# Performance work log

Hardware: AMD Instinct MI355X
Metric: run time of the kernel (lower is better)

## Reference

```python
import jax, jax.numpy as jnp
import numpy as np


def setup_inputs() -> dict:
    key = jax.random.key(0)
    ks = jax.random.split(key, 7)
    B, S = 64, 1024
    V, E, H, L, O = 128, 512, 512, 2, 256
    scale = 0.05
    return {
        "input_ids": jax.random.randint(ks[0], (B, S), 0, V),
        "emb": jax.random.normal(ks[1], (V, E), dtype=jnp.float32) * scale,
        "Wxh": jax.random.normal(ks[2], (L, H, E), dtype=jnp.float32) * scale,
        "Whh": jax.random.normal(ks[3], (L, H, H), dtype=jnp.float32) * scale,
        "bh": jax.random.normal(ks[4], (L, H), dtype=jnp.float32) * scale,
        "Why": jax.random.normal(ks[5], (O, H), dtype=jnp.float32) * scale,
        "by": jax.random.normal(ks[6], (O,), dtype=jnp.float32) * scale,
    }


def reference(input_ids, emb, Wxh, Whh, bh, Why, by):
    # input_ids: [B, S] int; emb: [V, E]; Wxh/Whh: [L, H, *]; bh: [L, H]
    L, H, _ = Wxh.shape
    B, S = input_ids.shape
    embedded = emb[input_ids]                 # [B, S, E]
    xs = jnp.swapaxes(embedded, 0, 1)         # [S, B, E] for scan over time
    h0 = jnp.zeros((L, B, H), dtype=embedded.dtype)

    def step(h, x_t):
        inp = x_t
        new_h = []
        for l in range(L):  # small fixed layer loop
            hn = jnp.tanh(inp @ Wxh[l].T + h[l] @ Whh[l].T + bh[l])
            new_h.append(hn)
            inp = hn
        return jnp.stack(new_h), inp          # carry [L,B,H], emit top layer [B,H]

    _, ys = jax.lax.scan(step, h0, xs)        # ys: [S, B, H]
    hidden_seq = jnp.swapaxes(ys, 0, 1)       # [B, S, H]
    return hidden_seq @ Why.T + by            # [B, S, O]
```

## Files before the change

kernel.cpp:

```cpp
#include <hip/hip_runtime.h>
#include <stdint.h>

#define B_ 64
#define S_ 1024
#define V_ 128
#define E_ 512
#define H_ 512
#define O_ 256
#define SLOTU 32768

typedef __attribute__((ext_vector_type(8))) short bf16x8;
typedef __attribute__((ext_vector_type(4))) float f32x4;
typedef __attribute__((ext_vector_type(4))) unsigned int u32x4;
typedef __attribute__((ext_vector_type(2))) unsigned int u32x2;
typedef unsigned short u16;
typedef unsigned int u32;

__device__ __forceinline__ u16 f2bf(float f) {
  unsigned u = __builtin_bit_cast(unsigned, f);
  u = u + 0x7FFFu + ((u >> 16) & 1u);
  return (u16)(u >> 16);
}
__device__ __forceinline__ float bf2f(u16 h) {
  unsigned u = ((unsigned)h) << 16;
  return __builtin_bit_cast(float, u);
}
__device__ __forceinline__ float fast_tanh(float x) {
  float a = __builtin_amdgcn_exp2f(x * 2.8853900817779268f);
  return 1.0f - 2.0f * __builtin_amdgcn_rcpf(a + 1.0f);
}
__device__ __forceinline__ u32 pk_hi(u32 a, u32 b) { return (a & 0xffffu) | (b << 16); }
__device__ __forceinline__ u32 pk_lo(u32 a, u32 b) { return (a >> 16) | (b & 0xffff0000u); }

__device__ __forceinline__ u32x4 ld_sc1_x4(const u32* p) {
  u32x4 v;
  asm volatile("global_load_dwordx4 %0, %1, off sc0 sc1" : "=v"(v) : "v"(p));
  return v;
}
__device__ __forceinline__ u32 ld_sc1_u32(const u32* p) {
  u32 v;
  asm volatile("global_load_dword %0, %1, off sc0 sc1" : "=v"(v) : "v"(p));
  return v;
}
__device__ __forceinline__ void st_sc1_u32(u32* p, u32 v) {
  asm volatile("global_store_dword %0, %1, off sc0 sc1" :: "v"(p), "v"(v) : "memory");
}
__device__ __forceinline__ void st_short_nt(u16* p, u32 v) {
  asm volatile("global_store_short %0, %1, off nt" :: "v"(p), "v"(v) : "memory");
}
__device__ __forceinline__ void vm0_fence() {
  asm volatile("s_waitcnt vmcnt(0)" ::: "memory");
  __builtin_amdgcn_sched_barrier(0);
}
__device__ __forceinline__ void poll4(const u32* p, u32 tgt) {
  for (;;) {
    u32x4 v;
    asm volatile("global_load_dwordx4 %0, %1, off sc0 sc1\n\ts_waitcnt vmcnt(0)"
                 : "=v"(v) : "v"(p) : "memory");
    if (v.x >= tgt && v.y >= tgt && v.z >= tgt && v.w >= tgt) return;
    __builtin_amdgcn_s_sleep(1);
  }
}

__global__ void k_embed(const float* __restrict__ emb, const float* __restrict__ Wxh0,
                        const float* __restrict__ bh0, float* __restrict__ EW0) {
  __shared__ float es[E_];
  const int v = blockIdx.x;
  for (int e = threadIdx.x; e < E_; e += blockDim.x) es[e] = emb[v * E_ + e];
  __syncthreads();
  for (int h = threadIdx.x; h < H_; h += blockDim.x) {
    const float* wr = Wxh0 + (size_t)h * E_;
    float acc = bh0[h];
    #pragma unroll 4
    for (int e = 0; e < E_; e += 4)
      acc += es[e] * wr[e] + es[e+1] * wr[e+1] + es[e+2] * wr[e+2] + es[e+3] * wr[e+3];
    EW0[(size_t)v * H_ + h] = acc;
  }
}

__global__ __launch_bounds__(512, 2) void k_pipe(
    const float* __restrict__ Whh, const float* __restrict__ Wxh,
    const int* __restrict__ ids, const float* __restrict__ EW0,
    const float* __restrict__ bh,
    u32* __restrict__ h0r,
    u32* __restrict__ x1r,
    u32* __restrict__ h1r,
    u16* __restrict__ h1full,
    u32* __restrict__ fa)
{
  __shared__ u32 lds_hi_w[2 * 4096];
  __shared__ u32 lds_lo_w[2 * 4096];

  const int tid  = threadIdx.x;
  const int wave = tid >> 6, lane = tid & 63;
  const int l15 = lane & 15, lhi = lane >> 4;
  const int bid = blockIdx.x;
  const int role = bid >> 4, sub = bid & 15;
  const int g = sub >> 2, cb = sub & 3;
  const int n = cb * 128 + wave * 16 + l15;
  const int goff = g * 16 * 512;

  u32* h0f = fa;
  u32* x1f = fa + 256;
  u32* h1f = fa + 512;

  const float* Wsel = (role == 0) ? Whh
                    : (role == 1) ? (Wxh + (size_t)H_ * H_)
                                  : (Whh + (size_t)H_ * H_);
  bf16x8 whi[16], wlo[16];
  {
    const float* wr = Wsel + (size_t)n * H_ + lhi * 8;
    #pragma unroll
    for (int ks = 0; ks < 16; ++ks) {
      const float* src = wr + ks * 32;
      bf16x8 h, l;
      #pragma unroll
      for (int j = 0; j < 8; ++j) {
        const float v = src[j];
        const u16 hb = f2bf(v);
        h[j] = (short)hb;
        l[j] = (short)f2bf(v - bf2f(hb));
      }
      whi[ks] = h; wlo[ks] = l;
    }
  }

  int aoff[16];
  {
    const int sw = l15 & 7;
    #pragma unroll
    for (int ks = 0; ks < 16; ++ks)
      aoff[ks] = l15 * 1024 + (((ks * 4 + lhi) ^ sw) << 4);
  }

  const int sr = tid >> 5, sm = tid & 31;
  auto stage_wr = [&](int buf, int cs, u32x4 q) {
    const int byte = buf * 16384 + sr * 1024 + (sm & 1) * 8 +
                     ((((cs << 4) + (sm >> 1)) ^ (sr & 7)) << 4);
    u32x2 hi = { pk_hi(q.x, q.y), pk_hi(q.z, q.w) };
    u32x2 lo = { pk_lo(q.x, q.y), pk_lo(q.z, q.w) };
    *(u32x2*)((char*)lds_hi_w + byte) = hi;
    *(u32x2*)((char*)lds_lo_w + byte) = lo;
  };
  auto stage3 = [&](const u32* base, int buf) {
    const u32* rowp = base + sr * 512 + sm * 4;
    const int c0 = (cb + 1) & 3, c1 = (cb + 2) & 3, c2 = (cb + 3) & 3;
    u32x4 q0 = ld_sc1_x4(rowp + c0 * 128);
    u32x4 q1 = ld_sc1_x4(rowp + c1 * 128);
    u32x4 q2 = ld_sc1_x4(rowp + c2 * 128);
    vm0_fence();
    stage_wr(buf, c0, q0); stage_wr(buf, c1, q1); stage_wr(buf, c2, q2);
  };
  auto stage4 = [&](const u32* base, int buf) {
    const u32* rowp = base + sr * 512 + sm * 4;
    u32x4 q0 = ld_sc1_x4(rowp);
    u32x4 q1 = ld_sc1_x4(rowp + 128);
    u32x4 q2 = ld_sc1_x4(rowp + 256);
    u32x4 q3 = ld_sc1_x4(rowp + 384);
    vm0_fence();
    stage_wr(buf, 0, q0); stage_wr(buf, 1, q1); stage_wr(buf, 2, q2); stage_wr(buf, 3, q3);
  };

  auto mm3 = [&](int buf, f32x4& out) {
    const char* bh_ = (const char*)lds_hi_w + buf * 16384;
    const char* bl_ = (const char*)lds_lo_w + buf * 16384;
    f32x4 c0 = {0.f,0.f,0.f,0.f}, c1 = c0, c2 = c0;
    #pragma unroll
    for (int ks = 0; ks < 16; ++ks) {
      bf16x8 ah = *(const bf16x8*)(bh_ + aoff[ks]);
      bf16x8 al = *(const bf16x8*)(bl_ + aoff[ks]);
      c0 = __builtin_amdgcn_mfma_f32_16x16x32_bf16(ah, whi[ks], c0, 0, 0, 0);
      c1 = __builtin_amdgcn_mfma_f32_16x16x32_bf16(al, whi[ks], c1, 0, 0, 0);
      c2 = __builtin_amdgcn_mfma_f32_16x16x32_bf16(ah, wlo[ks], c2, 0, 0, 0);
    }
    out = c0 + c1 + c2;
  };

  auto self_write = [&](int buf, const u16* hbv, const u16* lbv) {
    char* bh_ = (char*)lds_hi_w + buf * 16384;
    char* bl_ = (char*)lds_lo_w + buf * 16384;
    const int gcol = n >> 3, coff = (n & 7) * 2;
    #pragma unroll
    for (int j = 0; j < 4; ++j) {
      const int r = lhi * 4 + j;
      const int byte = r * 1024 + ((gcol ^ (r & 7)) << 4) + coff;
      *(u16*)(bh_ + byte) = hbv[j];
      *(u16*)(bl_ + byte) = lbv[j];
    }
  };

  if (role == 0) {
    for (int t = 0; t < S_; ++t) {
      float ew[4];
      #pragma unroll
      for (int j = 0; j < 4; ++j) {
        const int b = g * 16 + lhi * 4 + j;
        ew[j] = EW0[(size_t)ids[b * S_ + t] * H_ + n];
      }
      if (tid == 0) {
        if (t > 0) poll4(&h0f[((g << 4) | ((t - 1) & 15)) * 4], (u32)t);
        if ((t & 7) == 0 && t >= 16)
          poll4(&x1f[((g << 4) | ((t - 9) & 15)) * 4], (u32)(t - 8));
      }
      __syncthreads();
      const int cur = t & 1;
      f32x4 acc = {0.f,0.f,0.f,0.f};
      if (t > 0) {
        stage3(h0r + (size_t)((t - 1) & 15) * SLOTU + goff, cur);
        __syncthreads();
        mm3(cur, acc);
      }
      u32* wsl = h0r + (size_t)(t & 15) * SLOTU;
      u16 hbv[4], lbv[4];
      #pragma unroll
      for (int j = 0; j < 4; ++j) {
        const int b = g * 16 + lhi * 4 + j;
        const float h = fast_tanh(acc[j] + ew[j]);
        hbv[j] = f2bf(h);
        lbv[j] = f2bf(h - bf2f(hbv[j]));
        st_sc1_u32(wsl + (size_t)b * 512 + n, (u32)hbv[j] | ((u32)lbv[j] << 16));
      }
      self_write(cur ^ 1, hbv, lbv);
      vm0_fence();
      __syncthreads();
      if (tid == 0) st_sc1_u32(&h0f[((g << 4) | (t & 15)) * 4 + cb], (u32)(t + 1));
    }
  } else if (role == 1) {
    const float bias = bh[H_ + n];
    for (int t = 0; t < S_; ++t) {
      if (tid == 0) {
        poll4(&h0f[((g << 4) | (t & 15)) * 4], (u32)(t + 1));
        if ((t & 7) == 0 && t >= 16)
          poll4(&h1f[((g << 4) | ((t - 9) & 15)) * 4], (u32)(t - 8));
      }
      __syncthreads();
      const int cur = t & 1;
      stage4(h0r + (size_t)(t & 15) * SLOTU + goff, cur);
      __syncthreads();
      f32x4 acc;
      mm3(cur, acc);
      u32* xsl = x1r + (size_t)(t & 15) * SLOTU;
      #pragma unroll
      for (int j = 0; j < 4; ++j) {
        const int b = g * 16 + lhi * 4 + j;
        const float v = acc[j] + bias;
        st_sc1_u32(xsl + (size_t)b * 512 + n, __builtin_bit_cast(u32, v));
      }
      vm0_fence();
      __syncthreads();
      if (tid == 0) st_sc1_u32(&x1f[((g << 4) | (t & 15)) * 4 + cb], (u32)(t + 1));
    }
  } else {
    for (int t = 0; t < S_; ++t) {
      if (tid == 0) {
        poll4(&x1f[((g << 4) | (t & 15)) * 4], (u32)(t + 1));
        if (t > 0) poll4(&h1f[((g << 4) | ((t - 1) & 15)) * 4], (u32)t);
      }
      __syncthreads();
      const u32* xsl = x1r + (size_t)(t & 15) * SLOTU;
      u32 xv[4];
      #pragma unroll
      for (int j = 0; j < 4; ++j) {
        const int b = g * 16 + lhi * 4 + j;
        xv[j] = ld_sc1_u32(xsl + (size_t)b * 512 + n);
      }
      const int cur = t & 1;
      f32x4 acc = {0.f,0.f,0.f,0.f};
      if (t > 0) {
        stage3(h1r + (size_t)((t - 1) & 3) * SLOTU + goff, cur);
        __syncthreads();
        mm3(cur, acc);
        vm0_fence();
      } else {
        vm0_fence();
      }
      u32* wsl = h1r + (size_t)(t & 3) * SLOTU;
      u16 hbv[4], lbv[4];
      #pragma unroll
      for (int j = 0; j < 4; ++j) {
        const int b = g * 16 + lhi * 4 + j;
        const float h = fast_tanh(acc[j] + __builtin_bit_cast(float, xv[j]));
        hbv[j] = f2bf(h);
        lbv[j] = f2bf(h - bf2f(hbv[j]));
        st_sc1_u32(wsl + (size_t)b * 512 + n, (u32)hbv[j] | ((u32)lbv[j] << 16));
      }
      self_write(cur ^ 1, hbv, lbv);
      vm0_fence();
      __syncthreads();
      if (tid == 0) st_sc1_u32(&h1f[((g << 4) | (t & 15)) * 4 + cb], (u32)(t + 1));
      #pragma unroll
      for (int j = 0; j < 4; ++j) {
        const int b = g * 16 + lhi * 4 + j;
        st_short_nt(h1full + ((size_t)b * S_ + t) * H_ + n, (u32)hbv[j]);
      }
    }
  }
}

__global__ void k_gemm_out(const u16* __restrict__ A, const float* __restrict__ Bw,
                           const float* __restrict__ bias, float* __restrict__ outp) {
  const int tid  = threadIdx.x;
  const int wave = tid >> 6, lane = tid & 63;
  const int l15 = lane & 15, lhi = lane >> 4;
  const int M0  = blockIdx.x * 64;
  const int ncb = wave * 64;

  #pragma unroll
  for (int nt = 0; nt < 4; ++nt) {
    const int nn = ncb + nt * 16 + l15;
    const float* wr = Bw + (size_t)nn * H_ + lhi * 8;
    bf16x8 w[16];
    #pragma unroll
    for (int ks = 0; ks < 16; ++ks) {
      const float* src = wr + ks * 32;
      bf16x8 ww;
      #pragma unroll
      for (int j = 0; j < 8; ++j) ww[j] = (short)f2bf(src[j]);
      w[ks] = ww;
    }
    const float bs = bias[nn];
    for (int mi = 0; mi < 4; ++mi) {
      const int m0 = M0 + mi * 16;
      const u16* arow = A + ((size_t)(m0 + l15)) * H_ + lhi * 8;
      f32x4 acc = {0.f, 0.f, 0.f, 0.f};
      #pragma unroll
      for (int ks = 0; ks < 16; ++ks) {
        bf16x8 a = *(const bf16x8*)(arow + ks * 32);
        acc = __builtin_amdgcn_mfma_f32_16x16x32_bf16(a, w[ks], acc, 0, 0, 0);
      }
      #pragma unroll
      for (int j = 0; j < 4; ++j)
        outp[(size_t)(m0 + lhi * 4 + j) * O_ + nn] = acc[j] + bs;
    }
  }
}

extern "C" void kernel_launch(void* const* d_in, const int* in_sizes, int n_in,
                              void* d_out, int out_size, void* d_ws, size_t ws_size,
                              hipStream_t stream) {
  const int*   ids = (const int*)d_in[0];
  const float* emb = (const float*)d_in[1];
  const float* Wxh = (const float*)d_in[2];
  const float* Whh = (const float*)d_in[3];
  const float* bh  = (const float*)d_in[4];
  const float* Why = (const float*)d_in[5];
  const float* by  = (const float*)d_in[6];
  float* out = (float*)d_out;

  char* ws = (char*)d_ws;
  size_t off = 0;
  float* EW0  = (float*)(ws + off); off += (size_t)V_ * H_ * 4;
  u32* h0r    = (u32*)(ws + off);   off += (size_t)16 * SLOTU * 4;
  u32* x1r    = (u32*)(ws + off);   off += (size_t)16 * SLOTU * 4;
  u32* h1r    = (u32*)(ws + off);   off += (size_t)4 * SLOTU * 4;
  u32* fa     = (u32*)(ws + off);   off += 4096;
  u16* h1full = (u16*)(ws + off);   off += (size_t)B_ * S_ * H_ * 2;

  hipMemsetAsync(fa, 0, 4096, stream);

  k_embed<<<dim3(V_), dim3(256), 0, stream>>>(emb, Wxh, bh, EW0);

  k_pipe<<<dim3(48), dim3(512), 0, stream>>>(Whh, Wxh, ids, EW0, bh,
                                             h0r, x1r, h1r, h1full, fa);

  k_gemm_out<<<dim3((B_ * S_) / 64), dim3(256), 0, stream>>>(h1full, Why, by, out);
}
```

Before: 3.931 ms.

## Replace flag-based inter-block sync with per-element sequence tags on data

Each hidden-state element is now stored together with a step tag in a dwordx2, and consumers poll the data itself until every tag matches, instead of waiting on separate per-step flag words after a vmcnt fence and block barrier. This removes one round trip of flag store and flag poll per timestep in all three pipeline roles, and drops several __syncthreads. Coarse progress counters are kept only for ring-buffer backpressure, published every 8 steps. It also reorders the loops so the next step's state is staged right after this step's output. The cost is doubled ring-buffer traffic, a larger memset to clear the tags, and spin loops executed by every thread.

New measurement: 4.188 ms. +6.5%, slower.

```diff
diff --git a/kernel.cpp b/kernel.cpp
--- a/kernel.cpp
+++ b/kernel.cpp
@@ -7,7 +7,7 @@
 #define E_ 512
 #define H_ 512
 #define O_ 256
-#define SLOTU 32768
+#define PSLOT (B_ * H_ * 2)
 
 typedef __attribute__((ext_vector_type(8))) short bf16x8;
 typedef __attribute__((ext_vector_type(4))) float f32x4;
@@ -37,10 +37,14 @@
   asm volatile("global_load_dwordx4 %0, %1, off sc0 sc1" : "=v"(v) : "v"(p));
   return v;
 }
-__device__ __forceinline__ u32 ld_sc1_u32(const u32* p) {
-  u32 v;
-  asm volatile("global_load_dword %0, %1, off sc0 sc1" : "=v"(v) : "v"(p));
+__device__ __forceinline__ u32x2 ld_sc1_x2(const u32* p) {
+  u32x2 v;
+  asm volatile("global_load_dwordx2 %0, %1, off sc0 sc1" : "=v"(v) : "v"(p));
   return v;
+}
+__device__ __forceinline__ void st_sc1_x2(u32* p, u32 d, u32 tag) {
+  u32x2 v = {d, tag};
+  asm volatile("global_store_dwordx2 %0, %1, off sc0 sc1" :: "v"(p), "v"(v) : "memory");
 }
 __device__ __forceinline__ void st_sc1_u32(u32* p, u32 v) {
   asm volatile("global_store_dword %0, %1, off sc0 sc1" :: "v"(p), "v"(v) : "memory");
@@ -98,11 +102,9 @@
   const int role = bid >> 4, sub = bid & 15;
   const int g = sub >> 2, cb = sub & 3;
   const int n = cb * 128 + wave * 16 + l15;
-  const int goff = g * 16 * 512;
-
-  u32* h0f = fa;
-  u32* x1f = fa + 256;
-  u32* h1f = fa + 512;
+
+  u32* x1prog = fa;
+  u32* r2prog = fa + 16;
 
   const float* Wsel = (role == 0) ? Whh
                     : (role == 1) ? (Wxh + (size_t)H_ * H_)
@@ -134,31 +136,56 @@
   }
 
   const int sr = tid >> 5, sm = tid & 31;
-  auto stage_wr = [&](int buf, int cs, u32x4 q) {
+  const int rowbase = (g * 16 + sr) * 512;
+
+  auto wr_lds = [&](int buf, int cs, u32 d0, u32 d1, u32 d2, u32 d3) {
     const int byte = buf * 16384 + sr * 1024 + (sm & 1) * 8 +
                      ((((cs << 4) + (sm >> 1)) ^ (sr & 7)) << 4);
-    u32x2 hi = { pk_hi(q.x, q.y), pk_hi(q.z, q.w) };
-    u32x2 lo = { pk_lo(q.x, q.y), pk_lo(q.z, q.w) };
+    u32x2 hi = { pk_hi(d0, d1), pk_hi(d2, d3) };
+    u32x2 lo = { pk_lo(d0, d1), pk_lo(d2, d3) };
     *(u32x2*)((char*)lds_hi_w + byte) = hi;
     *(u32x2*)((char*)lds_lo_w + byte) = lo;
   };
-  auto stage3 = [&](const u32* base, int buf) {
-    const u32* rowp = base + sr * 512 + sm * 4;
+
+  auto pollstage3 = [&](const u32* slot, u32 want, int buf) {
     const int c0 = (cb + 1) & 3, c1 = (cb + 2) & 3, c2 = (cb + 3) & 3;
-    u32x4 q0 = ld_sc1_x4(rowp + c0 * 128);
-    u32x4 q1 = ld_sc1_x4(rowp + c1 * 128);
-    u32x4 q2 = ld_sc1_x4(rowp + c2 * 128);
-    vm0_fence();
-    stage_wr(buf, c0, q0); stage_wr(buf, c1, q1); stage_wr(buf, c2, q2);
+    const u32* p0 = slot + ((rowbase + c0 * 128 + sm * 4) << 1);
+    const u32* p1 = slot + ((rowbase + c1 * 128 + sm * 4) << 1);
+    const u32* p2 = slot + ((rowbase + c2 * 128 + sm * 4) << 1);
+    u32x4 a0, a1, b0, b1, d0, d1;
+    for (;;) {
+      a0 = ld_sc1_x4(p0); a1 = ld_sc1_x4(p0 + 4);
+      b0 = ld_sc1_x4(p1); b1 = ld_sc1_x4(p1 + 4);
+      d0 = ld_sc1_x4(p2); d1 = ld_sc1_x4(p2 + 4);
+      vm0_fence();
+      u32 bad = (a0.y ^ want) | (a0.w ^ want) | (a1.y ^ want) | (a1.w ^ want)
+              | (b0.y ^ want) | (b0.w ^ want) | (b1.y ^ want) | (b1.w ^ want)
+              | (d0.y ^ want) | (d0.w ^ want) | (d1.y ^ want) | (d1.w ^ want);
+      if (!bad) break;
+    }
+    wr_lds(buf, c0, a0.x, a0.z, a1.x, a1.z);
+    wr_lds(buf, c1, b0.x, b0.z, b1.x, b1.z);
+    wr_lds(buf, c2, d0.x, d0.z, d1.x, d1.z);
   };
-  auto stage4 = [&](const u32* base, int buf) {
-    const u32* rowp = base + sr * 512 + sm * 4;
-    u32x4 q0 = ld_sc1_x4(rowp);
-    u32x4 q1 = ld_sc1_x4(rowp + 128);
-    u32x4 q2 = ld_sc1_x4(rowp + 256);
-    u32x4 q3 = ld_sc1_x4(rowp + 384);
-    vm0_fence();
-    stage_wr(buf, 0, q0); stage_wr(buf, 1, q1); stage_wr(buf, 2, q2); stage_wr(buf, 3, q3);
+
+  auto pollstage4 = [&](const u32* slot, u32 want, int buf) {
+    const u32* p0 = slot + ((rowbase + sm * 4) << 1);
+    u32x4 q[8];
+    for (;;) {
+      #pragma unroll
+      for (int c = 0; c < 4; ++c) {
+        q[2*c]   = ld_sc1_x4(p0 + (c * 128 << 1));
+        q[2*c+1] = ld_sc1_x4(p0 + (c * 128 << 1) + 4);
+      }
+      vm0_fence();
+      u32 bad = 0;
+      #pragma unroll
+      for (int i = 0; i < 8; ++i) bad |= (q[i].y ^ want) | (q[i].w ^ want);
+      if (!bad) break;
+    }
+    #pragma unroll
+    for (int c = 0; c < 4; ++c)
+      wr_lds(buf, c, q[2*c].x, q[2*c].z, q[2*c+1].x, q[2*c+1].z);
   };
 
   auto mm3 = [&](int buf, f32x4& out) {
@@ -197,20 +224,10 @@
         const int b = g * 16 + lhi * 4 + j;
         ew[j] = EW0[(size_t)ids[b * S_ + t] * H_ + n];
       }
-      if (tid == 0) {
-        if (t > 0) poll4(&h0f[((g << 4) | ((t - 1) & 15)) * 4], (u32)t);
-        if ((t & 7) == 0 && t >= 16)
-          poll4(&x1f[((g << 4) | ((t - 9) & 15)) * 4], (u32)(t - 8));
-      }
-      __syncthreads();
       const int cur = t & 1;
       f32x4 acc = {0.f,0.f,0.f,0.f};
-      if (t > 0) {
-        stage3(h0r + (size_t)((t - 1) & 15) * SLOTU + goff, cur);
-        __syncthreads();
-        mm3(cur, acc);
-      }
-      u32* wsl = h0r + (size_t)(t & 15) * SLOTU;
+      if (t > 0) mm3(cur, acc);
+      u32* wsl = h0r + (size_t)(t & 15) * PSLOT;
       u16 hbv[4], lbv[4];
       #pragma unroll
       for (int j = 0; j < 4; ++j) {
@@ -218,81 +235,104 @@
         const float h = fast_tanh(acc[j] + ew[j]);
         hbv[j] = f2bf(h);
         lbv[j] = f2bf(h - bf2f(hbv[j]));
-        st_sc1_u32(wsl + (size_t)b * 512 + n, (u32)hbv[j] | ((u32)lbv[j] << 16));
+        st_sc1_x2(wsl + (((size_t)b * 512 + n) << 1),
+                  (u32)hbv[j] | ((u32)lbv[j] << 16), (u32)(t + 1));
       }
       self_write(cur ^ 1, hbv, lbv);
-      vm0_fence();
+      if ((t & 7) == 0 && t >= 16 && tid == 0) poll4(&x1prog[g * 4], (u32)(t - 8));
+      if (t + 1 < S_) pollstage3(wsl, (u32)(t + 1), cur ^ 1);
       __syncthreads();
-      if (tid == 0) st_sc1_u32(&h0f[((g << 4) | (t & 15)) * 4 + cb], (u32)(t + 1));
     }
   } else if (role == 1) {
     const float bias = bh[H_ + n];
     for (int t = 0; t < S_; ++t) {
-      if (tid == 0) {
-        poll4(&h0f[((g << 4) | (t & 15)) * 4], (u32)(t + 1));
-        if ((t & 7) == 0 && t >= 16)
-          poll4(&h1f[((g << 4) | ((t - 9) & 15)) * 4], (u32)(t - 8));
-      }
-      __syncthreads();
+      if ((t & 7) == 0 && t >= 16 && tid == 0) poll4(&r2prog[g * 4], (u32)(t - 8));
       const int cur = t & 1;
-      stage4(h0r + (size_t)(t & 15) * SLOTU + goff, cur);
+      pollstage4(h0r + (size_t)(t & 15) * PSLOT, (u32)(t + 1), cur);
       __syncthreads();
       f32x4 acc;
       mm3(cur, acc);
-      u32* xsl = x1r + (size_t)(t & 15) * SLOTU;
+      u32* xsl = x1r + (size_t)(t & 15) * PSLOT;
       #pragma unroll
       for (int j = 0; j < 4; ++j) {
         const int b = g * 16 + lhi * 4 + j;
         const float v = acc[j] + bias;
-        st_sc1_u32(xsl + (size_t)b * 512 + n, __builtin_bit_cast(u32, v));
-      }
-      vm0_fence();
-      __syncthreads();
-      if (tid == 0) st_sc1_u32(&x1f[((g << 4) | (t & 15)) * 4 + cb], (u32)(t + 1));
+        st_sc1_x2(xsl + (((size_t)b * 512 + n) << 1),
+                  __builtin_bit_cast(u32, v), (u32)(t + 1));
+      }
+      if ((t & 7) == 7 && tid == 0) st_sc1_u32(&x1prog[g * 4 + cb], (u32)(t + 1));
     }
   } else {
+    u32 xvb[4];
+    {
+      const u32* xsl = x1r;
+      u32x2 xq[4];
+      for (;;) {
+        #pragma unroll
+        for (int j = 0; j < 4; ++j) {
+          const int b = g * 16 + lhi * 4 + j;
+          xq[j] = ld_sc1_x2(xsl + (((size_t)b * 512 + n) << 1));
+        }
+        vm0_fence();
+        u32 bad = 0;
+        #pragma unroll
+        for (int j = 0; j < 4; ++j) bad |= xq[j].y ^ 1u;
+        if (!bad) break;
+      }
+      #pragma unroll
+      for (int j = 0; j < 4; ++j) xvb[j] = xq[j].x;
+    }
     for (int t = 0; t < S_; ++t) {
-      if (tid == 0) {
-        poll4(&x1f[((g << 4) | (t & 15)) * 4], (u32)(t + 1));
-        if (t > 0) poll4(&h1f[((g << 4) | ((t - 1) & 15)) * 4], (u32)t);
-      }
-      __syncthreads();
-      const u32* xsl = x1r + (size_t)(t & 15) * SLOTU;
-      u32 xv[4];
+      const int cur = t & 1;
+      f32x4 acc = {0.f,0.f,0.f,0.f};
+      if (t > 0) mm3(cur, acc);
+      u32* wsl = h1r + (size_t)(t & 3) * PSLOT;
+      u16 hbv[4], lbv[4];
       #pragma unroll
       for (int j = 0; j < 4; ++j) {
         const int b = g * 16 + lhi * 4 + j;
-        xv[j] = ld_sc1_u32(xsl + (size_t)b * 512 + n);
-      }
-      const int cur = t & 1;
-      f32x4 acc = {0.f,0.f,0.f,0.f};
-      if (t > 0) {
-        stage3(h1r + (size_t)((t - 1) & 3) * SLOTU + goff, cur);
-        __syncthreads();
-        mm3(cur, acc);
-        vm0_fence();
-      } else {
-        vm0_fence();
-      }
-      u32* wsl = h1r + (size_t)(t & 3) * SLOTU;
-      u16 hbv[4], lbv[4];
-      #pragma unroll
-      for (int j = 0; j < 4; ++j) {
-        const int b = g * 16 + lhi * 4 + j;
-        const float h = fast_tanh(acc[j] + __builtin_bit_cast(float, xv[j]));
+        const float h = fast_tanh(acc[j] + __builtin_bit_cast(float, xvb[j]));
         hbv[j] = f2bf(h);
         lbv[j] = f2bf(h - bf2f(hbv[j]));
-        st_sc1_u32(wsl + (size_t)b * 512 + n, (u32)hbv[j] | ((u32)lbv[j] << 16));
+        st_sc1_x2(wsl + (((size_t)b * 512 + n) << 1),
+                  (u32)hbv[j] | ((u32)lbv[j] << 16), (u32)(t + 1));
+        st_short_nt(h1full + ((size_t)b * S_ + t) * H_ + n, (u32)hbv[j]);
       }
       self_write(cur ^ 1, hbv, lbv);
-      vm0_fence();
+      if ((t & 7) == 7 && tid == 0) st_sc1_u32(&r2prog[g * 4 + cb], (u32)(t + 1));
+      if (t + 1 < S_) {
+        const u32 want = (u32)(t + 1), xwant = (u32)(t + 2);
+        const int c0 = (cb + 1) & 3, c1 = (cb + 2) & 3, c2 = (cb + 3) & 3;
+        const u32* p0 = wsl + ((rowbase + c0 * 128 + sm * 4) << 1);
+        const u32* p1 = wsl + ((rowbase + c1 * 128 + sm * 4) << 1);
+        const u32* p2 = wsl + ((rowbase + c2 * 128 + sm * 4) << 1);
+        const u32* xsl = x1r + (size_t)((t + 1) & 15) * PSLOT;
+        u32x4 a0, a1, b0, b1, d0, d1;
+        u32x2 xq[4];
+        for (;;) {
+          a0 = ld_sc1_x4(p0); a1 = ld_sc1_x4(p0 + 4);
+          b0 = ld_sc1_x4(p1); b1 = ld_sc1_x4(p1 + 4);
+          d0 = ld_sc1_x4(p2); d1 = ld_sc1_x4(p2 + 4);
+          #pragma unroll
+          for (int j = 0; j < 4; ++j) {
+            const int b = g * 16 + lhi * 4 + j;
+            xq[j] = ld_sc1_x2(xsl + (((size_t)b * 512 + n) << 1));
+          }
+          vm0_fence();
+          u32 bad = (a0.y ^ want) | (a0.w ^ want) | (a1.y ^ want) | (a1.w ^ want)
+                  | (b0.y ^ want) | (b0.w ^ want) | (b1.y ^ want) | (b1.w ^ want)
+                  | (d0.y ^ want) | (d0.w ^ want) | (d1.y ^ want) | (d1.w ^ want);
+          #pragma unroll
+          for (int j = 0; j < 4; ++j) bad |= xq[j].y ^ xwant;
+          if (!bad) break;
+        }
+        wr_lds(cur ^ 1, c0, a0.x, a0.z, a1.x, a1.z);
+        wr_lds(cur ^ 1, c1, b0.x, b0.z, b1.x, b1.z);
+        wr_lds(cur ^ 1, c2, d0.x, d0.z, d1.x, d1.z);
+        #pragma unroll
+        for (int j = 0; j < 4; ++j) xvb[j] = xq[j].x;
+      }
       __syncthreads();
-      if (tid == 0) st_sc1_u32(&h1f[((g << 4) | (t & 15)) * 4 + cb], (u32)(t + 1));
-      #pragma unroll
-      for (int j = 0; j < 4; ++j) {
-        const int b = g * 16 + lhi * 4 + j;
-        st_short_nt(h1full + ((size_t)b * S_ + t) * H_ + n, (u32)hbv[j]);
-      }
     }
   }
 }
@@ -350,13 +390,14 @@
   char* ws = (char*)d_ws;
   size_t off = 0;
   float* EW0  = (float*)(ws + off); off += (size_t)V_ * H_ * 4;
-  u32* h0r    = (u32*)(ws + off);   off += (size_t)16 * SLOTU * 4;
-  u32* x1r    = (u32*)(ws + off);   off += (size_t)16 * SLOTU * 4;
-  u32* h1r    = (u32*)(ws + off);   off += (size_t)4 * SLOTU * 4;
+  u32* h0r    = (u32*)(ws + off);   off += (size_t)16 * PSLOT * 4;
+  u32* x1r    = (u32*)(ws + off);   off += (size_t)16 * PSLOT * 4;
+  u32* h1r    = (u32*)(ws + off);   off += (size_t)4 * PSLOT * 4;
   u32* fa     = (u32*)(ws + off);   off += 4096;
   u16* h1full = (u16*)(ws + off);   off += (size_t)B_ * S_ * H_ * 2;
 
-  hipMemsetAsync(fa, 0, 4096, stream);
+  const size_t zlen = (size_t)(16 + 16 + 4) * PSLOT * 4 + 4096;
+  hipMemsetAsync(h0r, 0, zlen, stream);
 
   k_embed<<<dim3(V_), dim3(256), 0, stream>>>(emb, Wxh, bh, EW0);
 
```

## Replace per-step flag handshakes with phase bits embedded in data words

Applied to the files above, without the earlier changes.

The persistent pipeline kernel no longer uses a per-timestep flag written after a fence and polled by one thread. Each consumer instead spins directly on the data it needs, checking a phase bit stored in the LSB of the low-bf16 word (or of the fp32 x1 value). This removes a fence, a block barrier and a flag round trip from every step. Coarse progress counters every 8 steps still provide back-pressure for ring-buffer reuse. The cost is one bit of mantissa precision in the stored values, a larger memset to clear the ring buffers, and a risk of spinning on partially visible writes.

Result: faster. 3.598 ms (-8.5%).

```diff
diff --git a/kernel.cpp b/kernel.cpp
--- a/kernel.cpp
+++ b/kernel.cpp
@@ -98,11 +98,9 @@
   const int role = bid >> 4, sub = bid & 15;
   const int g = sub >> 2, cb = sub & 3;
   const int n = cb * 128 + wave * 16 + l15;
-  const int goff = g * 16 * 512;
-
-  u32* h0f = fa;
-  u32* x1f = fa + 256;
-  u32* h1f = fa + 512;
+
+  u32* x1prog = fa;
+  u32* r2prog = fa + 16;
 
   const float* Wsel = (role == 0) ? Whh
                     : (role == 1) ? (Wxh + (size_t)H_ * H_)
@@ -134,7 +132,9 @@
   }
 
   const int sr = tid >> 5, sm = tid & 31;
-  auto stage_wr = [&](int buf, int cs, u32x4 q) {
+  const int rowbase = (g * 16 + sr) * 512;
+
+  auto wr_lds = [&](int buf, int cs, u32x4 q) {
     const int byte = buf * 16384 + sr * 1024 + (sm & 1) * 8 +
                      ((((cs << 4) + (sm >> 1)) ^ (sr & 7)) << 4);
     u32x2 hi = { pk_hi(q.x, q.y), pk_hi(q.z, q.w) };
@@ -142,23 +142,38 @@
     *(u32x2*)((char*)lds_hi_w + byte) = hi;
     *(u32x2*)((char*)lds_lo_w + byte) = lo;
   };
-  auto stage3 = [&](const u32* base, int buf) {
-    const u32* rowp = base + sr * 512 + sm * 4;
+
+  auto pollstage3 = [&](const u32* slot, u32 ph16, int buf) {
     const int c0 = (cb + 1) & 3, c1 = (cb + 2) & 3, c2 = (cb + 3) & 3;
-    u32x4 q0 = ld_sc1_x4(rowp + c0 * 128);
-    u32x4 q1 = ld_sc1_x4(rowp + c1 * 128);
-    u32x4 q2 = ld_sc1_x4(rowp + c2 * 128);
-    vm0_fence();
-    stage_wr(buf, c0, q0); stage_wr(buf, c1, q1); stage_wr(buf, c2, q2);
-  };
-  auto stage4 = [&](const u32* base, int buf) {
-    const u32* rowp = base + sr * 512 + sm * 4;
-    u32x4 q0 = ld_sc1_x4(rowp);
-    u32x4 q1 = ld_sc1_x4(rowp + 128);
-    u32x4 q2 = ld_sc1_x4(rowp + 256);
-    u32x4 q3 = ld_sc1_x4(rowp + 384);
-    vm0_fence();
-    stage_wr(buf, 0, q0); stage_wr(buf, 1, q1); stage_wr(buf, 2, q2); stage_wr(buf, 3, q3);
+    const u32* p0 = slot + rowbase + c0 * 128 + sm * 4;
+    const u32* p1 = slot + rowbase + c1 * 128 + sm * 4;
+    const u32* p2 = slot + rowbase + c2 * 128 + sm * 4;
+    u32x4 a, b, d;
+    for (;;) {
+      a = ld_sc1_x4(p0); b = ld_sc1_x4(p1); d = ld_sc1_x4(p2);
+      vm0_fence();
+      u32 bad = ((a.x ^ ph16) | (a.y ^ ph16) | (a.z ^ ph16) | (a.w ^ ph16)
+               | (b.x ^ ph16) | (b.y ^ ph16) | (b.z ^ ph16) | (b.w ^ ph16)
+               | (d.x ^ ph16) | (d.y ^ ph16) | (d.z ^ ph16) | (d.w ^ ph16)) & 0x10000u;
+      if (!bad) break;
+    }
+    wr_lds(buf, c0, a); wr_lds(buf, c1, b); wr_lds(buf, c2, d);
+  };
+
+  auto pollstage4 = [&](const u32* slot, u32 ph16, int buf) {
+    const u32* p = slot + rowbase + sm * 4;
+    u32x4 q0, q1, q2, q3;
+    for (;;) {
+      q0 = ld_sc1_x4(p);       q1 = ld_sc1_x4(p + 128);
+      q2 = ld_sc1_x4(p + 256); q3 = ld_sc1_x4(p + 384);
+      vm0_fence();
+      u32 bad = ((q0.x ^ ph16) | (q0.y ^ ph16) | (q0.z ^ ph16) | (q0.w ^ ph16)
+               | (q1.x ^ ph16) | (q1.y ^ ph16) | (q1.z ^ ph16) | (q1.w ^ ph16)
+               | (q2.x ^ ph16) | (q2.y ^ ph16) | (q2.z ^ ph16) | (q2.w ^ ph16)
+               | (q3.x ^ ph16) | (q3.y ^ ph16) | (q3.z ^ ph16) | (q3.w ^ ph16)) & 0x10000u;
+      if (!bad) break;
+    }
+    wr_lds(buf, 0, q0); wr_lds(buf, 1, q1); wr_lds(buf, 2, q2); wr_lds(buf, 3, q3);
   };
 
   auto mm3 = [&](int buf, f32x4& out) {
@@ -190,26 +205,21 @@
   };
 
   if (role == 0) {
+    int cur = 0;
     for (int t = 0; t < S_; ++t) {
+      if ((t & 7) == 0 && t >= 16) {
+        if (tid == 0) poll4(&x1prog[g * 4], (u32)(t - 8));
+        __syncthreads();
+      }
       float ew[4];
       #pragma unroll
       for (int j = 0; j < 4; ++j) {
         const int b = g * 16 + lhi * 4 + j;
         ew[j] = EW0[(size_t)ids[b * S_ + t] * H_ + n];
       }
-      if (tid == 0) {
-        if (t > 0) poll4(&h0f[((g << 4) | ((t - 1) & 15)) * 4], (u32)t);
-        if ((t & 7) == 0 && t >= 16)
-          poll4(&x1f[((g << 4) | ((t - 9) & 15)) * 4], (u32)(t - 8));
-      }
-      __syncthreads();
-      const int cur = t & 1;
       f32x4 acc = {0.f,0.f,0.f,0.f};
-      if (t > 0) {
-        stage3(h0r + (size_t)((t - 1) & 15) * SLOTU + goff, cur);
-        __syncthreads();
-        mm3(cur, acc);
-      }
+      if (t > 0) mm3(cur, acc);
+      const u32 ph = (((u32)t >> 4) & 1u) ^ 1u;
       u32* wsl = h0r + (size_t)(t & 15) * SLOTU;
       u16 hbv[4], lbv[4];
       #pragma unroll
@@ -217,25 +227,24 @@
         const int b = g * 16 + lhi * 4 + j;
         const float h = fast_tanh(acc[j] + ew[j]);
         hbv[j] = f2bf(h);
-        lbv[j] = f2bf(h - bf2f(hbv[j]));
+        lbv[j] = (u16)((f2bf(h - bf2f(hbv[j])) & 0xFFFEu) | ph);
         st_sc1_u32(wsl + (size_t)b * 512 + n, (u32)hbv[j] | ((u32)lbv[j] << 16));
       }
       self_write(cur ^ 1, hbv, lbv);
-      vm0_fence();
+      if (t + 1 < S_) pollstage3(wsl, ph << 16, cur ^ 1);
       __syncthreads();
-      if (tid == 0) st_sc1_u32(&h0f[((g << 4) | (t & 15)) * 4 + cb], (u32)(t + 1));
+      cur ^= 1;
     }
   } else if (role == 1) {
     const float bias = bh[H_ + n];
+    int cur = 0;
     for (int t = 0; t < S_; ++t) {
-      if (tid == 0) {
-        poll4(&h0f[((g << 4) | (t & 15)) * 4], (u32)(t + 1));
-        if ((t & 7) == 0 && t >= 16)
-          poll4(&h1f[((g << 4) | ((t - 9) & 15)) * 4], (u32)(t - 8));
-      }
-      __syncthreads();
-      const int cur = t & 1;
-      stage4(h0r + (size_t)(t & 15) * SLOTU + goff, cur);
+      if ((t & 7) == 0 && t >= 16) {
+        if (tid == 0) poll4(&r2prog[g * 4], (u32)(t - 8));
+        __syncthreads();
+      }
+      const u32 ph = (((u32)t >> 4) & 1u) ^ 1u;
+      pollstage4(h0r + (size_t)(t & 15) * SLOTU, ph << 16, cur);
       __syncthreads();
       f32x4 acc;
       mm3(cur, acc);
@@ -243,56 +252,76 @@
       #pragma unroll
       for (int j = 0; j < 4; ++j) {
         const int b = g * 16 + lhi * 4 + j;
-        const float v = acc[j] + bias;
-        st_sc1_u32(xsl + (size_t)b * 512 + n, __builtin_bit_cast(u32, v));
-      }
-      vm0_fence();
-      __syncthreads();
-      if (tid == 0) st_sc1_u32(&x1f[((g << 4) | (t & 15)) * 4 + cb], (u32)(t + 1));
+        const u32 w = (__builtin_bit_cast(u32, acc[j] + bias) & ~1u) | ph;
+        st_sc1_u32(xsl + (size_t)b * 512 + n, w);
+      }
+      if ((t & 7) == 7 && tid == 0)
+        st_sc1_u32(&x1prog[g * 4 + cb], (u32)(t + 1));
+      cur ^= 1;
     }
   } else {
+    u32 xvb[4];
+    {
+      u32 x0, x1v, x2, x3;
+      for (;;) {
+        const int b = g * 16 + lhi * 4;
+        x0 = ld_sc1_u32(x1r + (size_t)b * 512 + n);
+        x1v = ld_sc1_u32(x1r + (size_t)(b + 1) * 512 + n);
+        x2 = ld_sc1_u32(x1r + (size_t)(b + 2) * 512 + n);
+        x3 = ld_sc1_u32(x1r + (size_t)(b + 3) * 512 + n);
+        vm0_fence();
+        if (((x0 & x1v & x2 & x3) & 1u) == 1u) break;
+      }
+      xvb[0] = x0; xvb[1] = x1v; xvb[2] = x2; xvb[3] = x3;
+    }
+    int cur = 0;
     for (int t = 0; t < S_; ++t) {
-      if (tid == 0) {
-        poll4(&x1f[((g << 4) | (t & 15)) * 4], (u32)(t + 1));
-        if (t > 0) poll4(&h1f[((g << 4) | ((t - 1) & 15)) * 4], (u32)t);
-      }
-      __syncthreads();
-      const u32* xsl = x1r + (size_t)(t & 15) * SLOTU;
-      u32 xv[4];
+      f32x4 acc = {0.f,0.f,0.f,0.f};
+      if (t > 0) mm3(cur, acc);
+      const u32 ph1 = (((u32)t >> 2) & 1u) ^ 1u;
+      u32* wsl = h1r + (size_t)(t & 3) * SLOTU;
+      u16 hbv[4], lbv[4];
       #pragma unroll
       for (int j = 0; j < 4; ++j) {
         const int b = g * 16 + lhi * 4 + j;
-        xv[j] = ld_sc1_u32(xsl + (size_t)b * 512 + n);
-      }
-      const int cur = t & 1;
-      f32x4 acc = {0.f,0.f,0.f,0.f};
-      if (t > 0) {
-        stage3(h1r + (size_t)((t - 1) & 3) * SLOTU + goff, cur);
-        __syncthreads();
-        mm3(cur, acc);
-        vm0_fence();
-      } else {
-        vm0_fence();
-      }
-      u32* wsl = h1r + (size_t)(t & 3) * SLOTU;
-      u16 hbv[4], lbv[4];
-      #pragma unroll
-      for (int j = 0; j < 4; ++j) {
-        const int b = g * 16 + lhi * 4 + j;
-        const float h = fast_tanh(acc[j] + __builtin_bit_cast(float, xv[j]));
+        const float h = fast_tanh(acc[j] + __builtin_bit_cast(float, xvb[j]));
         hbv[j] = f2bf(h);
-        lbv[j] = f2bf(h - bf2f(hbv[j]));
+        lbv[j] = (u16)((f2bf(h - bf2f(hbv[j])) & 0xFFFEu) | ph1);
         st_sc1_u32(wsl + (size_t)b * 512 + n, (u32)hbv[j] | ((u32)lbv[j] << 16));
+        st_short_nt(h1full + ((size_t)b * S_ + t) * H_ + n, (u32)hbv[j]);
       }
       self_write(cur ^ 1, hbv, lbv);
-      vm0_fence();
+      if ((t & 7) == 7 && tid == 0)
+        st_sc1_u32(&r2prog[g * 4 + cb], (u32)(t + 1));
+      if (t + 1 < S_) {
+        const u32 ph16 = ph1 << 16;
+        const u32 phx = ((((u32)(t + 1)) >> 4) & 1u) ^ 1u;
+        const int c0 = (cb + 1) & 3, c1 = (cb + 2) & 3, c2 = (cb + 3) & 3;
+        const u32* p0 = wsl + rowbase + c0 * 128 + sm * 4;
+        const u32* p1 = wsl + rowbase + c1 * 128 + sm * 4;
+        const u32* p2 = wsl + rowbase + c2 * 128 + sm * 4;
+        const u32* xsl = x1r + (size_t)((t + 1) & 15) * SLOTU;
+        const int b0 = g * 16 + lhi * 4;
+        u32x4 a, b, d;
+        u32 x0, x1v, x2, x3;
+        for (;;) {
+          a = ld_sc1_x4(p0); b = ld_sc1_x4(p1); d = ld_sc1_x4(p2);
+          x0 = ld_sc1_u32(xsl + (size_t)b0 * 512 + n);
+          x1v = ld_sc1_u32(xsl + (size_t)(b0 + 1) * 512 + n);
+          x2 = ld_sc1_u32(xsl + (size_t)(b0 + 2) * 512 + n);
+          x3 = ld_sc1_u32(xsl + (size_t)(b0 + 3) * 512 + n);
+          vm0_fence();
+          u32 bad = ((a.x ^ ph16) | (a.y ^ ph16) | (a.z ^ ph16) | (a.w ^ ph16)
+                   | (b.x ^ ph16) | (b.y ^ ph16) | (b.z ^ ph16) | (b.w ^ ph16)
+                   | (d.x ^ ph16) | (d.y ^ ph16) | (d.z ^ ph16) | (d.w ^ ph16)) & 0x10000u;
+          bad |= ((x0 ^ phx) | (x1v ^ phx) | (x2 ^ phx) | (x3 ^ phx)) & 1u;
+          if (!bad) break;
+        }
+        wr_lds(cur ^ 1, c0, a); wr_lds(cur ^ 1, c1, b); wr_lds(cur ^ 1, c2, d);
+        xvb[0] = x0; xvb[1] = x1v; xvb[2] = x2; xvb[3] = x3;
+      }
       __syncthreads();
-      if (tid == 0) st_sc1_u32(&h1f[((g << 4) | (t & 15)) * 4 + cb], (u32)(t + 1));
-      #pragma unroll
-      for (int j = 0; j < 4; ++j) {
-        const int b = g * 16 + lhi * 4 + j;
-        st_short_nt(h1full + ((size_t)b * S_ + t) * H_ + n, (u32)hbv[j]);
-      }
+      cur ^= 1;
     }
   }
 }
@@ -356,7 +385,8 @@
   u32* fa     = (u32*)(ws + off);   off += 4096;
   u16* h1full = (u16*)(ws + off);   off += (size_t)B_ * S_ * H_ * 2;
 
-  hipMemsetAsync(fa, 0, 4096, stream);
+  const size_t zlen = (size_t)(16 + 16 + 4) * SLOTU * 4 + 4096;
+  hipMemsetAsync(h0r, 0, zlen, stream);
 
   k_embed<<<dim3(V_), dim3(256), 0, stream>>>(emb, Wxh, bh, EW0);
 
```
